# Performance work log

Measured on AMD Instinct MI355X. Metric: run time of the kernel, lower is better.

## Reference

```python
import jax, jax.numpy as jnp
import numpy as np

B, T, V, E, H = 256, 512, 30000, 256, 32


def _run_dir(x, mask, Wih, Whh, bih, bhh, reverse):
    # x: [B,T,D], mask: [B,T] bool. PyTorch GRU gate order: r, z, n.
    gi = jnp.einsum('btd,gd->btg', x, Wih) + bih  # precompute input gates [B,T,3H]
    h0 = jnp.zeros((x.shape[0], Whh.shape[1]), x.dtype)

    def step(h, inp):
        gi_t, m_t = inp
        gh = h @ Whh.T + bhh
        ir, iz, inn = jnp.split(gi_t, 3, axis=-1)
        hr, hz, hn = jnp.split(gh, 3, axis=-1)
        r = jax.nn.sigmoid(ir + hr)
        z = jax.nn.sigmoid(iz + hz)
        n = jnp.tanh(inn + r * hn)
        h_new = (1.0 - z) * n + z * h
        # packed-sequence semantics: freeze state at padded steps
        h = jnp.where(m_t[:, None], h_new, h)
        return h, h

    hT, ys = jax.lax.scan(step, h0, (jnp.swapaxes(gi, 0, 1), mask.T), reverse=reverse)
    return jnp.swapaxes(ys, 0, 1), hT  # outputs [B,T,H], final hidden [B,H]


def _bigru_layer(x, mask, pf, pb):
    of, hf = _run_dir(x, mask, *pf, reverse=False)
    ob, hb = _run_dir(x, mask, *pb, reverse=True)
    return jnp.concatenate([of, ob], axis=-1), hf, hb


def setup_inputs() -> dict:
    key = jax.random.key(0)
    ks = jax.random.split(key, 24)
    lengths = jax.random.randint(ks[0], (B,), 1, T + 1)
    mask = (jnp.arange(T)[None, :] < lengths[:, None]).astype(jnp.int32)
    ids = jax.random.randint(ks[1], (B, T), 1, V)
    ids = jnp.where(mask > 0, ids, 0)  # pad_id = 0 at padded positions
    embed = (jax.random.normal(ks[2], (V, E), jnp.float32) * 0.1).at[0].set(0.0)

    def gru_params(k, din):
        k1, k2, k3, k4 = jax.random.split(k, 4)
        s = 1.0 / np.sqrt(H)
        return (jax.random.uniform(k1, (3 * H, din), jnp.float32, -s, s),
                jax.random.uniform(k2, (3 * H, H), jnp.float32, -s, s),
                jax.random.uniform(k3, (3 * H,), jnp.float32, -s, s),
                jax.random.uniform(k4, (3 * H,), jnp.float32, -s, s))

    inp = {"input_ids": ids, "attention_mask": mask, "embed": embed}
    i = 3
    for layer, din in (("l0", E), ("l1", 2 * H)):
        for d in ("f", "b"):
            Wih, Whh, bih, bhh = gru_params(ks[i], din); i += 1
            inp[f"Wih_{layer}{d}"] = Wih
            inp[f"Whh_{layer}{d}"] = Whh
            inp[f"bih_{layer}{d}"] = bih
            inp[f"bhh_{layer}{d}"] = bhh
    s = 1.0 / np.sqrt(2 * H)
    inp["Wout"] = jax.random.uniform(ks[i], (6, 2 * H), jnp.float32, -s, s)
    inp["bout"] = jax.random.uniform(ks[i + 1], (6,), jnp.float32, -s, s)
    return inp


def reference(input_ids, attention_mask, embed,
              Wih_l0f, Whh_l0f, bih_l0f, bhh_l0f,
              Wih_l0b, Whh_l0b, bih_l0b, bhh_l0b,
              Wih_l1f, Whh_l1f, bih_l1f, bhh_l1f,
              Wih_l1b, Whh_l1b, bih_l1b, bhh_l1b,
              Wout, bout):
    mask = attention_mask > 0
    x = embed[input_ids]  # [B,T,E]
    x1, _, _ = _bigru_layer(x, mask,
                            (Wih_l0f, Whh_l0f, bih_l0f, bhh_l0f),
                            (Wih_l0b, Whh_l0b, bih_l0b, bhh_l0b))
    # no dropout: eval-mode forward
    _, hf, hb = _bigru_layer(x1, mask,
                             (Wih_l1f, Whh_l1f, bih_l1f, bhh_l1f),
                             (Wih_l1b, Whh_l1b, bih_l1b, bhh_l1b))
    top = jnp.concatenate([hf, hb], axis=-1)  # h_n[-2:] -> [B, 2H]
    return top @ Wout.T + bout  # [B, 6]
```

## Files before the change

### kernel.cpp

```cpp
#include <hip/hip_runtime.h>
#include <hip/hip_bf16.h>
#include <stdint.h>

#define B_ 256
#define T_ 512
#define V_ 30000
#define E_ 256
#define H_ 32

typedef float v2f __attribute__((ext_vector_type(2)));
typedef unsigned int uint2e __attribute__((ext_vector_type(2)));

#define LOG2E_F 1.44269504088896340736f

__device__ __forceinline__ float exp2_fast(float x) {
    float r; asm("v_exp_f32 %0, %1" : "=v"(r) : "v"(x)); return r;
}
__device__ __forceinline__ float rcp_fast(float x) {
    float r; asm("v_rcp_f32 %0, %1" : "=v"(r) : "v"(x)); return r;
}
__device__ __forceinline__ void pk_fma(v2f& acc, v2f w, v2f h) {
    asm("v_pk_fma_f32 %0, %1, %2, %0" : "+v"(acc) : "v"(w), "v"(h));
}
template <int CTRL>
__device__ __forceinline__ float mdpp(float x) {
    return __int_as_float(
        __builtin_amdgcn_mov_dpp(__float_as_int(x), CTRL, 0xF, 0xF, true));
}
#define DPP_XOR1  0xB1
#define DPP_XOR2  0x4E
#define DPP_XOR3  0x1B
#define DPP_XOR7  0x141
#define DPP_XOR15 0x140

__device__ __forceinline__ float swap32(float x) {
    uint2e r = __builtin_amdgcn_permlane32_swap(
        __float_as_uint(x), __float_as_uint(x), false, false);
    return __uint_as_float(r.x ^ r.y ^ __float_as_uint(x));
}
__device__ __forceinline__ float swap16(float x) {
    uint2e r = __builtin_amdgcn_permlane16_swap(
        __float_as_uint(x), __float_as_uint(x), false, false);
    return __uint_as_float(r.x ^ r.y ^ __float_as_uint(x));
}

#define GEMM_MT 64
#define GEMM_KC 32
#define GEMM_PA 68
#define GEMM_PB 196

__global__ __launch_bounds__(256) void gemm_gates(
    const float* __restrict__ A, int M, int K,
    const float* __restrict__ Wf, const float* __restrict__ Wb,
    const float* __restrict__ bihf, const float* __restrict__ bhhf,
    const float* __restrict__ bihb, const float* __restrict__ bhhb,
    float* __restrict__ Out)
{
    __shared__ float As[GEMM_KC][GEMM_PA];
    __shared__ float Bs[GEMM_KC][GEMM_PB];

    const int tid = threadIdx.x;
    const int mbase = blockIdx.x * GEMM_MT;
    const int mg = tid >> 5, ng = tid & 31;
    const int m_off = mg * 8, n_off = ng * 6;

    float acc[8][6];
    #pragma unroll
    for (int r = 0; r < 8; ++r)
        #pragma unroll
        for (int c = 0; c < 6; ++c) acc[r][c] = 0.f;

    for (int kc = 0; kc < K; kc += GEMM_KC) {
        #pragma unroll
        for (int i = 0; i < 2; ++i) {
            int fi = tid + 256 * i;
            int row = fi >> 3, cf = fi & 7;
            int m = mbase + row;
            float4 v = make_float4(0.f, 0.f, 0.f, 0.f);
            if (m < M) v = *(const float4*)&A[(size_t)m * K + kc + cf * 4];
            As[cf * 4 + 0][row] = v.x; As[cf * 4 + 1][row] = v.y;
            As[cf * 4 + 2][row] = v.z; As[cf * 4 + 3][row] = v.w;
        }
        #pragma unroll
        for (int i = 0; i < 6; ++i) {
            int fi = tid + 256 * i;
            int g = fi >> 3, cf = fi & 7;
            const float* Wsel = (g < 96) ? (Wf + (size_t)g * K)
                                         : (Wb + (size_t)(g - 96) * K);
            float4 v = *(const float4*)&Wsel[kc + cf * 4];
            Bs[cf * 4 + 0][g] = v.x; Bs[cf * 4 + 1][g] = v.y;
            Bs[cf * 4 + 2][g] = v.z; Bs[cf * 4 + 3][g] = v.w;
        }
        __syncthreads();
        #pragma unroll
        for (int k = 0; k < GEMM_KC; ++k) {
            float a[8], bb[6];
            *(float4*)&a[0] = *(const float4*)&As[k][m_off];
            *(float4*)&a[4] = *(const float4*)&As[k][m_off + 4];
            *(float2*)&bb[0] = *(const float2*)&Bs[k][n_off];
            *(float2*)&bb[2] = *(const float2*)&Bs[k][n_off + 2];
            *(float2*)&bb[4] = *(const float2*)&Bs[k][n_off + 4];
            #pragma unroll
            for (int r = 0; r < 8; ++r)
                #pragma unroll
                for (int c = 0; c < 6; ++c)
                    acc[r][c] = fmaf(a[r], bb[c], acc[r][c]);
        }
        __syncthreads();
    }

    float bias[6], gsc[6];
    #pragma unroll
    for (int c = 0; c < 6; ++c) {
        int g = n_off + c;
        int g96 = (g < 96) ? g : g - 96;
        const float* bih = (g < 96) ? bihf : bihb;
        const float* bhh = (g < 96) ? bhhf : bhhb;
        bias[c] = bih[g96] + ((g96 < 64) ? bhh[g96] : 0.f);
        gsc[c]  = (g96 < 64) ? -LOG2E_F : 2.0f * LOG2E_F;
    }
    #pragma unroll
    for (int r = 0; r < 8; ++r) {
        int m = mbase + m_off + r;
        if (m < M) {
            float* op = &Out[(size_t)m * 192 + n_off];
            #pragma unroll
            for (int c = 0; c < 6; ++c) op[c] = (acc[r][c] + bias[c]) * gsc[c];
        }
    }
}

template <int USE_IDS>
__global__ __launch_bounds__(64, 1)
__attribute__((amdgpu_waves_per_eu(1, 1)))
void gru_scan(
    const float* __restrict__ gi,
    const int* __restrict__ ids,
    const int* __restrict__ mask,
    const float* __restrict__ Whh_f, const float* __restrict__ Whh_b,
    const float* __restrict__ bhh_f, const float* __restrict__ bhh_b,
    float* __restrict__ out_seq,
    float* __restrict__ out_fin)
{
    const int l = threadIdx.x;
    const int i16 = l & 15;
    const int row = l >> 4;
    const int hi = row & 1;
    const int kh = row >> 1;
    const int j = i16 + 16 * hi;
    const bool lower = l < 32;
    const bool self_seed = (hi == kh);
    const int dir = blockIdx.x & 1;
    const int b = blockIdx.x >> 1;
    const int bT = b * T_;

    const float* Whh = dir ? Whh_b : Whh_f;
    const float* bhh = dir ? bhh_b : bhh_f;

    const float sRZ = -LOG2E_F;
    const float sN2 = 2.0f * LOG2E_F;

    const int M0[8] = {0, 2, 7, 5, 15, 13, 8, 10};
    const int M1[8] = {1, 3, 6, 4, 14, 12, 9, 11};

    v2f wR[8], wZ[8], wN[8];
    #pragma unroll
    for (int q = 0; q < 8; ++q) {
        const int c0 = kh * 16 + (i16 ^ M0[q]);
        const int c1 = kh * 16 + (i16 ^ M1[q]);
        wR[q] = (v2f){Whh[j * 32 + c0] * sRZ, Whh[j * 32 + c1] * sRZ};
        wZ[q] = (v2f){Whh[(32 + j) * 32 + c0] * sRZ,
                      Whh[(32 + j) * 32 + c1] * sRZ};
        wN[q] = (v2f){Whh[(64 + j) * 32 + c0] * sN2,
                      Whh[(64 + j) * 32 + c1] * sN2};
    }
    float bns = bhh[64 + j] * sN2;

    #pragma unroll
    for (int q = 0; q < 8; ++q)
        asm volatile("" : "+v"(wR[q]), "+v"(wZ[q]), "+v"(wN[q]));
    asm volatile("" : "+v"(bns));

    const int offR = dir * 96 + j;
    const int offZ = dir * 96 + 32 + j;
    const int offN = dir * 96 + 64 + j;

    auto wbase = [&](int c) { return dir ? (bT + 508 - 4 * c) : (bT + 4 * c); };

    int4 ids0 = make_int4(0, 0, 0, 0);
    if (USE_IDS) ids0 = *(const int4*)&ids[wbase(0)];
    int4 mask_use = *(const int4*)&mask[wbase(0)];
    int4 mask_mid = *(const int4*)&mask[wbase(1)];
    int4 mask_in  = make_int4(0, 0, 0, 0);
    int4 ids_pf = make_int4(0, 0, 0, 0), ids_mid = ids_pf, ids_in = ids_pf;
    if (USE_IDS) {
        ids_pf  = *(const int4*)&ids[wbase(1)];
        ids_mid = *(const int4*)&ids[wbase(2)];
    }

    float gR[2][4], gZ[2][4], gN[2][4];
    #pragma unroll
    for (int u = 0; u < 4; ++u) {
        int rowi;
        if (USE_IDS) {
            const int* ip = (const int*)&ids0;
            rowi = dir ? ip[3 - u] : ip[u];
        } else {
            rowi = bT + (dir ? (511 - u) : u);
        }
        const float* gp = gi + (size_t)rowi * 192;
        gR[0][u] = gp[offR];
        gZ[0][u] = gp[offZ];
        gN[0][u] = gp[offN];
    }

    float h = 0.f;

    for (int c2 = 0; c2 < 64; ++c2) {
        #pragma unroll
        for (int pb = 0; pb < 2; ++pb) {
            const int c = 2 * c2 + pb;
            if (USE_IDS) {
                const int ci = (c + 3 < 128) ? (c + 3) : 127;
                ids_in = *(const int4*)&ids[wbase(ci)];
            }
            {
                const int cm = (c + 2 < 128) ? (c + 2) : 127;
                mask_in = *(const int4*)&mask[wbase(cm)];
            }
            const int cN = (c + 1 < 128) ? (c + 1) : 127;

            #pragma unroll
            for (int u = 0; u < 4; ++u) {
                int rowN;
                if (USE_IDS) {
                    const int* ip = (const int*)&ids_pf;
                    rowN = dir ? ip[3 - u] : ip[u];
                } else {
                    rowN = bT + (dir ? (511 - 4 * cN - u) : (4 * cN + u));
                }
                const float* gpN = gi + (size_t)rowN * 192;
                gR[pb ^ 1][u] = gpN[offR];
                gZ[pb ^ 1][u] = gpN[offZ];
                gN[pb ^ 1][u] = gpN[offN];

                const int* mu = (const int*)&mask_use;
                const int m = dir ? mu[3 - u] : mu[u];

                const float hx = swap16(h);
                const float seed = self_seed ? h : hx;

                v2f p[8];
                p[0].x = seed;                      p[0].y = mdpp<DPP_XOR1>(seed);
                p[1].x = mdpp<DPP_XOR2>(seed);      p[1].y = mdpp<DPP_XOR3>(seed);
                p[2].x = mdpp<DPP_XOR7>(seed);      p[2].y = mdpp<DPP_XOR7>(p[0].y);
                p[3].x = mdpp<DPP_XOR7>(p[1].x);    p[3].y = mdpp<DPP_XOR7>(p[1].y);
                p[4].x = mdpp<DPP_XOR15>(seed);     p[4].y = mdpp<DPP_XOR15>(p[0].y);
                p[5].x = mdpp<DPP_XOR15>(p[1].x);   p[5].y = mdpp<DPP_XOR15>(p[1].y);
                p[6].x = mdpp<DPP_XOR15>(p[2].x);   p[6].y = mdpp<DPP_XOR15>(p[2].y);
                p[7].x = mdpp<DPP_XOR15>(p[3].x);   p[7].y = mdpp<DPP_XOR15>(p[3].y);

                v2f aR = {0.f, 0.f}, aZ = {0.f, 0.f}, aN = {0.f, 0.f};
                #pragma unroll
                for (int q = 0; q < 8; ++q) {
                    pk_fma(aR, wR[q], p[q]);
                    pk_fma(aZ, wZ[q], p[q]);
                    pk_fma(aN, wN[q], p[q]);
                }
                const float sR = aR.x + aR.y;
                const float sZ = aZ.x + aZ.y;
                const float sN = aN.x + aN.y;
                const float SR = sR + swap32(sR);
                const float SZ = sZ + swap32(sZ);
                const float SN = sN + swap32(sN);

                const float yr  = gR[pb][u] + SR;
                const float yz  = gZ[pb][u] + SZ;
                const float hns = bns + SN;
                const float r = rcp_fast(1.0f + exp2_fast(yr));
                const float z = rcp_fast(1.0f + exp2_fast(yz));
                const float yn = gN[pb][u] + r * hns;
                const float n = fmaf(-2.0f, rcp_fast(1.0f + exp2_fast(yn)), 1.0f);
                const float hnew = n + z * (h - n);
                h = m ? hnew : h;

                if (out_seq != nullptr) {
                    const int t = dir ? (511 - 4 * c - u) : (4 * c + u);
                    if (lower)
                        out_seq[(size_t)(bT + t) * 64 + dir * 32 + j] = h;
                }
            }
            mask_use = mask_mid; mask_mid = mask_in;
            if (USE_IDS) { ids_pf = ids_mid; ids_mid = ids_in; }
        }
    }

    if (out_fin != nullptr && lower)
        out_fin[b * 64 + dir * 32 + j] = h;
}

__global__ void head_kernel(const float* __restrict__ hfin,
                            const float* __restrict__ Wout,
                            const float* __restrict__ bout,
                            float* __restrict__ out)
{
    int idx = blockIdx.x * blockDim.x + threadIdx.x;
    if (idx >= B_ * 6) return;
    int b = idx / 6, o = idx % 6;
    float acc = bout[o];
    const float* hp = hfin + b * 64;
    const float* wp = Wout + o * 64;
    #pragma unroll
    for (int k = 0; k < 64; ++k) acc = fmaf(hp[k], wp[k], acc);
    out[idx] = acc;
}

extern "C" void kernel_launch(void* const* d_in, const int* in_sizes, int n_in,
                              void* d_out, int out_size, void* d_ws, size_t ws_size,
                              hipStream_t stream)
{
    const int*   ids   = (const int*)d_in[0];
    const int*   mask  = (const int*)d_in[1];
    const float* embed = (const float*)d_in[2];
    const float* Wih0f = (const float*)d_in[3];
    const float* Whh0f = (const float*)d_in[4];
    const float* bih0f = (const float*)d_in[5];
    const float* bhh0f = (const float*)d_in[6];
    const float* Wih0b = (const float*)d_in[7];
    const float* Whh0b = (const float*)d_in[8];
    const float* bih0b = (const float*)d_in[9];
    const float* bhh0b = (const float*)d_in[10];
    const float* Wih1f = (const float*)d_in[11];
    const float* Whh1f = (const float*)d_in[12];
    const float* bih1f = (const float*)d_in[13];
    const float* bhh1f = (const float*)d_in[14];
    const float* Wih1b = (const float*)d_in[15];
    const float* Whh1b = (const float*)d_in[16];
    const float* bih1b = (const float*)d_in[17];
    const float* bhh1b = (const float*)d_in[18];
    const float* Wout  = (const float*)d_in[19];
    const float* bout  = (const float*)d_in[20];

    float* ws   = (float*)d_ws;
    float* gbuf = ws;
    float* x1   = ws + (size_t)B_ * T_ * 192;
    float* hfin = x1 + (size_t)B_ * T_ * 64;

    gemm_gates<<<(V_ + GEMM_MT - 1) / GEMM_MT, 256, 0, stream>>>(
        embed, V_, E_, Wih0f, Wih0b, bih0f, bhh0f, bih0b, bhh0b, gbuf);

    gru_scan<1><<<2 * B_, 64, 0, stream>>>(
        gbuf, ids, mask, Whh0f, Whh0b, bhh0f, bhh0b, x1, nullptr);

    gemm_gates<<<(B_ * T_) / GEMM_MT, 256, 0, stream>>>(
        x1, B_ * T_, 64, Wih1f, Wih1b, bih1f, bhh1f, bih1b, bhh1b, gbuf);

    gru_scan<0><<<2 * B_, 64, 0, stream>>>(
        gbuf, nullptr, mask, Whh1f, Whh1b, bhh1f, bhh1b, nullptr, hfin);

    head_kernel<<<(B_ * 6 + 255) / 256, 256, 0, stream>>>(hfin, Wout, bout,
                                                          (float*)d_out);
}
```

Baseline: 482.4 us.

## Stage GRU input gates per 32-step segment through LDS with coalesced float4 prefetch

Replaces the per-step scalar global loads of the precomputed input gates with segment-wise staging. Each 32-timestep segment is fetched with coalesced float4 loads into registers, written to a double-buffered LDS array, and read per step from LDS. Masks become a per-segment ballot bitmask instead of int4 loads every four steps. This takes global-memory latency off the serial recurrence critical path, at the cost of LDS traffic, extra registers for the 12 float4 prefetches, and a block of stores between segments.

```diff
diff --git a/kernel.cpp b/kernel.cpp
--- a/kernel.cpp
+++ b/kernel.cpp
@@ -7,6 +7,9 @@
 #define V_ 30000
 #define E_ 256
 #define H_ 32
+
+#define SEG 32
+#define NSEG (T_ / SEG)
 
 typedef float v2f __attribute__((ext_vector_type(2)));
 typedef unsigned int uint2e __attribute__((ext_vector_type(2)));
@@ -142,6 +145,9 @@
     float* __restrict__ out_seq,
     float* __restrict__ out_fin)
 {
+    __shared__ float g_lds[2][SEG][96];
+    __shared__ int   row_lds[2][SEG];
+
     const int l = threadIdx.x;
     const int i16 = l & 15;
     const int row = l >> 4;
@@ -181,71 +187,74 @@
         asm volatile("" : "+v"(wR[q]), "+v"(wZ[q]), "+v"(wN[q]));
     asm volatile("" : "+v"(bns));
 
-    const int offR = dir * 96 + j;
-    const int offZ = dir * 96 + 32 + j;
-    const int offN = dir * 96 + 64 + j;
-
-    auto wbase = [&](int c) { return dir ? (bT + 508 - 4 * c) : (bT + 4 * c); };
-
-    int4 ids0 = make_int4(0, 0, 0, 0);
-    if (USE_IDS) ids0 = *(const int4*)&ids[wbase(0)];
-    int4 mask_use = *(const int4*)&mask[wbase(0)];
-    int4 mask_mid = *(const int4*)&mask[wbase(1)];
-    int4 mask_in  = make_int4(0, 0, 0, 0);
-    int4 ids_pf = make_int4(0, 0, 0, 0), ids_mid = ids_pf, ids_in = ids_pf;
-    if (USE_IDS) {
-        ids_pf  = *(const int4*)&ids[wbase(1)];
-        ids_mid = *(const int4*)&ids[wbase(2)];
-    }
-
-    float gR[2][4], gZ[2][4], gN[2][4];
-    #pragma unroll
-    for (int u = 0; u < 4; ++u) {
-        int rowi;
-        if (USE_IDS) {
-            const int* ip = (const int*)&ids0;
-            rowi = dir ? ip[3 - u] : ip[u];
-        } else {
-            rowi = bT + (dir ? (511 - u) : u);
-        }
-        const float* gp = gi + (size_t)rowi * 192;
-        gR[0][u] = gp[offR];
-        gZ[0][u] = gp[offZ];
-        gN[0][u] = gp[offN];
-    }
+    auto t_of = [&](int n) { return dir ? (T_ - 1 - n) : n; };
+
+    uint32_t mseg_cur, mseg_nx1, mseg_nx2 = 0;
+    {
+        int mk0 = 0, mk1 = 0, rm0 = 0, rm1 = 0;
+        if (lower) {
+            const int ga0 = bT + t_of(l);
+            const int ga1 = bT + t_of(SEG + l);
+            mk0 = mask[ga0];
+            mk1 = mask[ga1];
+            if (USE_IDS) { rm0 = ids[ga0]; rm1 = ids[ga1]; }
+            else         { rm0 = ga0;      rm1 = ga1;      }
+        }
+        mseg_cur = (uint32_t)__ballot(lower && (mk0 != 0));
+        mseg_nx1 = (uint32_t)__ballot(lower && (mk1 != 0));
+        if (lower) { row_lds[0][l] = rm0; row_lds[1][l] = rm1; }
+
+        #pragma unroll
+        for (int i = 0; i < 12; ++i) {
+            const int f = l + 64 * i;
+            const int su = f / 24;
+            const int o4 = (f % 24) * 4;
+            const int rown = row_lds[0][su];
+            float4 v = *(const float4*)&gi[(size_t)rown * 192 + dir * 96 + o4];
+            *(float4*)&g_lds[0][su][o4] = v;
+        }
+    }
+    float cR = g_lds[0][0][j];
+    float cZ = g_lds[0][0][32 + j];
+    float cN = g_lds[0][0][64 + j];
 
     float h = 0.f;
 
-    for (int c2 = 0; c2 < 64; ++c2) {
-        #pragma unroll
-        for (int pb = 0; pb < 2; ++pb) {
-            const int c = 2 * c2 + pb;
-            if (USE_IDS) {
-                const int ci = (c + 3 < 128) ? (c + 3) : 127;
-                ids_in = *(const int4*)&ids[wbase(ci)];
+    for (int s = 0; s < NSEG; ++s) {
+        const int buf = s & 1;
+
+        int mk_r = 0, rm_r = 0;
+        if (s < NSEG - 2 && lower) {
+            const int ga = bT + t_of(SEG * (s + 2) + l);
+            mk_r = mask[ga];
+            if (USE_IDS) rm_r = ids[ga];
+            else         rm_r = ga;
+        }
+
+        float4 gv[12];
+        if (s < NSEG - 1) {
+            #pragma unroll
+            for (int i = 0; i < 12; ++i) {
+                const int f = l + 64 * i;
+                const int su = f / 24;
+                const int o4 = (f % 24) * 4;
+                int rown;
+                if (USE_IDS) rown = row_lds[buf ^ 1][su];
+                else         rown = bT + t_of(SEG * (s + 1) + su);
+                gv[i] = *(const float4*)&gi[(size_t)rown * 192 + dir * 96 + o4];
             }
-            {
-                const int cm = (c + 2 < 128) ? (c + 2) : 127;
-                mask_in = *(const int4*)&mask[wbase(cm)];
-            }
-            const int cN = (c + 1 < 128) ? (c + 1) : 127;
-
+        }
+        asm volatile("" ::: "memory");
+
+        const uint32_t mseg = mseg_cur;
+        for (int su4 = 0; su4 < 8; ++su4) {
             #pragma unroll
             for (int u = 0; u < 4; ++u) {
-                int rowN;
-                if (USE_IDS) {
-                    const int* ip = (const int*)&ids_pf;
-                    rowN = dir ? ip[3 - u] : ip[u];
-                } else {
-                    rowN = bT + (dir ? (511 - 4 * cN - u) : (4 * cN + u));
-                }
-                const float* gpN = gi + (size_t)rowN * 192;
-                gR[pb ^ 1][u] = gpN[offR];
-                gZ[pb ^ 1][u] = gpN[offZ];
-                gN[pb ^ 1][u] = gpN[offN];
-
-                const int* mu = (const int*)&mask_use;
-                const int m = dir ? mu[3 - u] : mu[u];
+                const int su = su4 * 4 + u;
+                const int sup = (su + 1 <= 31) ? (su + 1) : 31;
+                const float nR = g_lds[buf][sup][j];
+                const float nZ = g_lds[buf][sup][32 + j];
+                const float nN = g_lds[buf][sup][64 + j];
 
                 const float hx = swap16(h);
                 const float seed = self_seed ? h : hx;
@@ -274,24 +283,44 @@
                 const float SZ = sZ + swap32(sZ);
                 const float SN = sN + swap32(sN);
 
-                const float yr  = gR[pb][u] + SR;
-                const float yz  = gZ[pb][u] + SZ;
+                const float yr  = cR + SR;
+                const float yz  = cZ + SZ;
                 const float hns = bns + SN;
                 const float r = rcp_fast(1.0f + exp2_fast(yr));
                 const float z = rcp_fast(1.0f + exp2_fast(yz));
-                const float yn = gN[pb][u] + r * hns;
+                const float yn = cN + r * hns;
                 const float n = fmaf(-2.0f, rcp_fast(1.0f + exp2_fast(yn)), 1.0f);
                 const float hnew = n + z * (h - n);
-                h = m ? hnew : h;
-
-                if (out_seq != nullptr) {
-                    const int t = dir ? (511 - 4 * c - u) : (4 * c + u);
-                    if (lower)
-                        out_seq[(size_t)(bT + t) * 64 + dir * 32 + j] = h;
+                const bool mm = (mseg >> su) & 1u;
+                h = mm ? hnew : h;
+
+                if (out_seq != nullptr && lower) {
+                    const int t = t_of(SEG * s + su);
+                    out_seq[(size_t)(bT + t) * 64 + dir * 32 + j] = h;
                 }
+                cR = nR; cZ = nZ; cN = nN;
             }
-            mask_use = mask_mid; mask_mid = mask_in;
-            if (USE_IDS) { ids_pf = ids_mid; ids_mid = ids_in; }
+        }
+
+        if (s < NSEG - 1) {
+            #pragma unroll
+            for (int i = 0; i < 12; ++i) {
+                const int f = l + 64 * i;
+                const int su = f / 24;
+                const int o4 = (f % 24) * 4;
+                *(float4*)&g_lds[buf ^ 1][su][o4] = gv[i];
+            }
+        }
+        if (s < NSEG - 2) {
+            mseg_nx2 = (uint32_t)__ballot(lower && (mk_r != 0));
+            if (lower) row_lds[buf][l] = rm_r;
+        }
+        mseg_cur = mseg_nx1; mseg_nx1 = mseg_nx2;
+
+        if (s < NSEG - 1) {
+            cR = g_lds[buf ^ 1][0][j];
+            cZ = g_lds[buf ^ 1][0][32 + j];
+            cN = g_lds[buf ^ 1][0][64 + j];
         }
     }
 
```

Measured after the change: 499.8 us. 1.04x slower.
